# Optimization experiments

Hardware: AMD Instinct MI355X
Metric: run time of the kernel (lower is better)

The kernel has to match this reference:

```python
import jax, jax.numpy as jnp
import numpy as np


def setup_inputs() -> dict:
    key = jax.random.key(0)
    ks = jax.random.split(key, 16)
    B, T, A, R, M, D = 128, 1024, 512, 1024, 256, 256  # batch, max_time, annot, rnn, memory, attn dims
    F, K = 32, 31  # location filters, kernel size
    s = jnp.float32(0.02)
    return dict(
        memory=jax.random.normal(ks[0], (B, M), jnp.float32),
        context=jax.random.normal(ks[1], (B, A), jnp.float32),
        rnn_state=jax.random.normal(ks[2], (B, R), jnp.float32),
        annots=jax.random.normal(ks[3], (B, T, A), jnp.float32),
        atten=jax.random.uniform(ks[4], (B, 2, T), jnp.float32),
        mask=jax.random.randint(ks[5], (B, T), 0, 2).astype(jnp.int32),
        Wi=jax.random.normal(ks[6], (3 * R, A + M), jnp.float32) * s,   # GRU input weights (r,z,n)
        Wh=jax.random.normal(ks[7], (3 * R, R), jnp.float32) * s,       # GRU hidden weights
        bi=jnp.zeros((3 * R,), jnp.float32),
        bh=jnp.zeros((3 * R,), jnp.float32),
        conv_w=jax.random.normal(ks[8], (F, 2, K), jnp.float32) * s,    # loc_conv (OIH)
        loc_w=jax.random.normal(ks[9], (D, F), jnp.float32) * s,
        loc_b=jnp.zeros((D,), jnp.float32),
        q_w=jax.random.normal(ks[10], (D, R), jnp.float32) * s,
        q_b=jnp.zeros((D,), jnp.float32),
        a_w=jax.random.normal(ks[11], (D, A), jnp.float32) * s,
        a_b=jnp.zeros((D,), jnp.float32),
        v_w=jax.random.normal(ks[12], (1, D), jnp.float32) * s,
    )


def reference(memory, context, rnn_state, annots, atten, mask,
              Wi, Wh, bi, bh, conv_w, loc_w, loc_b, q_w, q_b, a_w, a_b, v_w):
    # --- GRUCell (torch gate order: r, z, n) ---
    x = jnp.concatenate([memory, context], axis=-1)          # (B, M+A)
    gi = x @ Wi.T + bi                                        # (B, 3R)
    gh = rnn_state @ Wh.T + bh                                # (B, 3R)
    ir, iz, inn = jnp.split(gi, 3, axis=-1)
    hr, hz, hn = jnp.split(gh, 3, axis=-1)
    r = jax.nn.sigmoid(ir + hr)
    z = jax.nn.sigmoid(iz + hz)
    n = jnp.tanh(inn + r * hn)
    h = (1.0 - z) * n + z * rnn_state                         # (B, R) rnn_output

    # --- Location-sensitive attention ---
    pad = (conv_w.shape[-1] - 1) // 2
    loc = jax.lax.conv_general_dilated(atten, conv_w, (1,), [(pad, pad)],
                                       dimension_numbers=('NCH', 'OIH', 'NCH'))  # (B, F, T)
    ploc = jnp.einsum('bft,df->btd', loc, loc_w) + loc_b      # (B, T, D)
    pq = (h @ q_w.T + q_b)[:, None, :]                        # (B, 1, D)
    pa = jnp.einsum('bta,da->btd', annots, a_w) + a_b         # (B, T, D)
    align = jnp.einsum('btd,d->bt', jnp.tanh(pq + pa + ploc), v_w[0])  # (B, T)

    # masked softmax (mask==0 -> -inf)
    align = jnp.where(mask != 0, align, jnp.float32(-1e30))
    align = jax.nn.softmax(align, axis=-1)

    # context = bmm(align, annots)
    ctx = jnp.einsum('bt,bta->ba', align, annots)             # (B, A)
    return (h, ctx, align)
```

## Files before the change

kernel.cpp:

```cpp
#include <hip/hip_runtime.h>
#include <cstddef>

constexpr int B  = 128;
constexpr int T  = 1024;
constexpr int AD = 512;
constexpr int R  = 1024;
constexpr int M  = 256;
constexpr int DD = 256;
constexpr int F  = 32;
constexpr int KW = 31;
constexpr int PADW = 15;
constexpr int XDIM = M + AD;
constexpr int G3 = 3 * R;
constexpr size_t BG3 = (size_t)B * G3;

using short8 = __attribute__((ext_vector_type(8))) short;
using f32x4  = __attribute__((ext_vector_type(4))) float;

__device__ __forceinline__ float sigmoidf(float x) { return 1.f / (1.f + __expf(-x)); }

__device__ __forceinline__ unsigned short f2bf(float x) {
  unsigned int u = __float_as_uint(x);
  u += 0x7FFFu + ((u >> 16) & 1u);
  return (unsigned short)(u >> 16);
}

__device__ __forceinline__ float tanh_fast(float x) {
  float e = __expf(2.f * x);
  return 1.f - 2.f / (e + 1.f);
}

__device__ __forceinline__ void load_lds16(const void* g, void* l) {
  __builtin_amdgcn_global_load_lds(
      (const __attribute__((address_space(1))) unsigned int*)g,
      (__attribute__((address_space(3))) unsigned int*)l, 16, 0, 0);
}

__global__ __launch_bounds__(256) void prep_wsw(const float* __restrict__ aw,
                                                const float* __restrict__ lw,
                                                unsigned short* __restrict__ awsw,
                                                unsigned short* __restrict__ lwsw) {
  int idx = blockIdx.x * 256 + threadIdx.x;
  int chunk = idx >> 10;
  int rn = (idx & 1023) >> 2;
  int u = idx & 3;
  int su = u ^ ((rn >> 1) & 3);
  const float* src;
  unsigned short* dst;
  if (chunk < 16) {
    src = aw + (size_t)rn * AD + chunk * 32 + u * 8;
    dst = awsw + chunk * 8192 + rn * 32 + su * 8;
  } else {
    src = lw + (size_t)rn * F + u * 8;
    dst = lwsw + rn * 32 + su * 8;
  }
  float4 f0 = *(const float4*)src;
  float4 f1 = *(const float4*)(src + 4);
  unsigned int w0 = f2bf(f0.x) | ((unsigned)f2bf(f0.y) << 16);
  unsigned int w1 = f2bf(f0.z) | ((unsigned)f2bf(f0.w) << 16);
  unsigned int w2 = f2bf(f1.x) | ((unsigned)f2bf(f1.y) << 16);
  unsigned int w3 = f2bf(f1.z) | ((unsigned)f2bf(f1.w) << 16);
  uint4 pk = {w0, w1, w2, w3};
  *(uint4*)dst = pk;
}

__global__ __launch_bounds__(256) void build_x(const float* __restrict__ mem,
                                               const float* __restrict__ ctx,
                                               float* __restrict__ x) {
  int idx = blockIdx.x * 256 + threadIdx.x;
  int b = idx / XDIM, k = idx - b * XDIM;
  x[idx] = (k < M) ? mem[(size_t)b * M + k] : ctx[(size_t)b * AD + (k - M)];
}

__global__ __launch_bounds__(256) void loc_conv(const float* __restrict__ atten,
                                                const float* __restrict__ conv_w,
                                                unsigned short* __restrict__ locw) {
  __shared__ float s_att[2 * 94];
  __shared__ float s_cw[F * 62];
  const int tid = threadIdx.x;
  const int t0 = blockIdx.x * 64, b = blockIdx.y;
  for (int i = tid; i < 2 * 94; i += 256) {
    int c = i / 94, ii = i - c * 94;
    int gt = t0 - PADW + ii;
    s_att[i] = (gt >= 0 && gt < T) ? atten[((size_t)b * 2 + c) * T + gt] : 0.f;
  }
  for (int i = tid; i < F * 62; i += 256) s_cw[i] = conv_w[i];
  __syncthreads();
  const int f = tid & 31;
  const int tb = (tid >> 5) * 8;
  float a8[8] = {0.f, 0.f, 0.f, 0.f, 0.f, 0.f, 0.f, 0.f};
#pragma unroll
  for (int c = 0; c < 2; ++c) {
    float win[38];
#pragma unroll
    for (int i = 0; i < 38; ++i) win[i] = s_att[c * 94 + tb + i];
#pragma unroll
    for (int k = 0; k < KW; ++k) {
      float w = s_cw[f * 62 + c * 31 + k];
#pragma unroll
      for (int ti = 0; ti < 8; ++ti) a8[ti] += w * win[ti + k];
    }
  }
#pragma unroll
  for (int ti = 0; ti < 8; ++ti)
    locw[((size_t)b * T + t0 + tb + ti) * F + f] = f2bf(a8[ti]);
}

__global__ __launch_bounds__(256) void gemm_fused(const float* __restrict__ x,
                                                  const float* __restrict__ rnn,
                                                  const float* __restrict__ Wi,
                                                  const float* __restrict__ Wh,
                                                  float* __restrict__ outp) {
  __shared__ __align__(16) float sX[16 * 68];
  __shared__ __align__(16) float sW[16 * 68];
  const int which = blockIdx.z >> 1, half = blockIdx.z & 1;
  const float* __restrict__ X = which ? rnn : x;
  const float* __restrict__ W = which ? Wh : Wi;
  const int K = which ? R : XDIM;
  const int Kh = K >> 1;
  const int kbeg = half * Kh, kend = kbeg + Kh;
  float* __restrict__ C = outp + (size_t)blockIdx.z * BG3;
  const int tid = threadIdx.x;
  const int g0 = blockIdx.x * 64, b0 = blockIdx.y * 64;
  const int bg = tid & 15, gg = tid >> 4;
  const int lr = tid >> 2, c4 = (tid & 3) * 4;
  float acc[4][4] = {};
  for (int k0 = kbeg; k0 < kend; k0 += 16) {
    float4 xv = *(const float4*)&X[(size_t)(b0 + lr) * K + k0 + c4];
    float4 wv = *(const float4*)&W[(size_t)(g0 + lr) * K + k0 + c4];
    sX[(c4 + 0) * 68 + lr] = xv.x; sX[(c4 + 1) * 68 + lr] = xv.y;
    sX[(c4 + 2) * 68 + lr] = xv.z; sX[(c4 + 3) * 68 + lr] = xv.w;
    sW[(c4 + 0) * 68 + lr] = wv.x; sW[(c4 + 1) * 68 + lr] = wv.y;
    sW[(c4 + 2) * 68 + lr] = wv.z; sW[(c4 + 3) * 68 + lr] = wv.w;
    __syncthreads();
#pragma unroll
    for (int k = 0; k < 16; ++k) {
      float4 xr = *(const float4*)&sX[k * 68 + bg * 4];
      float4 wr = *(const float4*)&sW[k * 68 + gg * 4];
      float xa[4] = {xr.x, xr.y, xr.z, xr.w};
      float wa[4] = {wr.x, wr.y, wr.z, wr.w};
#pragma unroll
      for (int ib = 0; ib < 4; ++ib)
#pragma unroll
        for (int jg = 0; jg < 4; ++jg) acc[ib][jg] += xa[ib] * wa[jg];
    }
    __syncthreads();
  }
#pragma unroll
  for (int ib = 0; ib < 4; ++ib) {
    float4 o;
    o.x = acc[ib][0]; o.y = acc[ib][1]; o.z = acc[ib][2]; o.w = acc[ib][3];
    *(float4*)&C[(size_t)(b0 + bg * 4 + ib) * G3 + g0 + gg * 4] = o;
  }
}

__global__ __launch_bounds__(256) void gru_combine(const float* __restrict__ gp,
                                                   const float* __restrict__ bi,
                                                   const float* __restrict__ bh,
                                                   const float* __restrict__ hprev,
                                                   float* __restrict__ hout) {
  int idx = blockIdx.x * 256 + threadIdx.x;
  int b = idx >> 10, j = idx & (R - 1);
  const float* gi0 = gp + (size_t)b * G3;
  const float* gi1 = gi0 + BG3;
  const float* gh0 = gi0 + 2 * BG3;
  const float* gh1 = gi0 + 3 * BG3;
  float ir = gi0[j] + gi1[j] + bi[j];
  float hr = gh0[j] + gh1[j] + bh[j];
  float iz = gi0[R + j] + gi1[R + j] + bi[R + j];
  float hz = gh0[R + j] + gh1[R + j] + bh[R + j];
  float inn = gi0[2 * R + j] + gi1[2 * R + j] + bi[2 * R + j];
  float hn = gh0[2 * R + j] + gh1[2 * R + j] + bh[2 * R + j];
  float r = sigmoidf(ir + hr);
  float z = sigmoidf(iz + hz);
  float n = tanhf(inn + r * hn);
  float hp = hprev[(size_t)b * R + j];
  hout[(size_t)b * R + j] = (1.f - z) * n + z * hp;
}

__global__ __launch_bounds__(256) void pq_kernel(const float* __restrict__ h,
                                                 const float* __restrict__ q_w,
                                                 const float* __restrict__ q_b,
                                                 float* __restrict__ pq) {
  __shared__ __align__(16) float sh[R];
  int b = blockIdx.x, tid = threadIdx.x;
  ((float4*)sh)[tid] = ((const float4*)(h + (size_t)b * R))[tid];
  __syncthreads();
  const float* wr = q_w + (size_t)tid * R;
  float acc = 0.f;
#pragma unroll 4
  for (int k = 0; k < R; k += 4) {
    float4 w = *(const float4*)&wr[k];
    float4 x = *(const float4*)&sh[k];
    acc += w.x * x.x + w.y * x.y + w.z * x.z + w.w * x.w;
  }
  pq[(size_t)b * DD + tid] = acc + q_b[tid];
}

__global__ __launch_bounds__(512, 4) void attn_energy_mfma(
    const float* __restrict__ annots, const unsigned short* __restrict__ locw,
    const int* __restrict__ mask,
    const unsigned short* __restrict__ awsw, const unsigned short* __restrict__ lwsw,
    const float* __restrict__ loc_b, const float* __restrict__ a_b,
    const float* __restrict__ v_w, const float* __restrict__ pq,
    float* __restrict__ align_out) {
  __shared__ __align__(16) unsigned short s_A[2][128 * 32];
  __shared__ __align__(16) unsigned short s_B[2][256 * 32];

  const int tid = threadIdx.x;
  const int wv = tid >> 6;
  const int wr = wv >> 2;
  const int wc = wv & 3;
  const int lane = tid & 63;
  const int lm = lane & 15;
  const int lg = lane >> 4;
  const int t0 = blockIdx.x * 128;
  const int b = blockIdx.y;
  const int suf = lg ^ ((lm >> 1) & 3);
  const int ar = tid >> 2, au = tid & 3;
  const int asu = au ^ ((ar >> 1) & 3);

  {
    float4 f0, f1;
    const float* gp = annots + ((size_t)b * T + t0 + ar) * AD + au * 8;
    f0 = *(const float4*)gp;
    f1 = *(const float4*)(gp + 4);
    load_lds16(awsw + (size_t)wv * 1024 + lane * 8, &s_B[0][wv * 1024]);
    load_lds16(awsw + (size_t)wv * 1024 + 512 + lane * 8, &s_B[0][wv * 1024 + 512]);
    unsigned int w0 = f2bf(f0.x) | ((unsigned)f2bf(f0.y) << 16);
    unsigned int w1 = f2bf(f0.z) | ((unsigned)f2bf(f0.w) << 16);
    unsigned int w2 = f2bf(f1.x) | ((unsigned)f2bf(f1.y) << 16);
    unsigned int w3 = f2bf(f1.z) | ((unsigned)f2bf(f1.w) << 16);
    uint4 pk = {w0, w1, w2, w3};
    *(uint4*)&s_A[0][ar * 32 + asu * 8] = pk;
  }

  f32x4 acc[4][4];
#pragma unroll
  for (int j = 0; j < 4; ++j) {
    int d = wc * 64 + j * 16 + lm;
    float base = pq[(size_t)b * DD + d] + a_b[d] + loc_b[d];
    f32x4 bv = {base, base, base, base};
#pragma unroll
    for (int i = 0; i < 4; ++i) acc[i][j] = bv;
  }
  __syncthreads();

#pragma unroll 1
  for (int ks = 0; ks < 17; ++ks) {
    const int cur = ks & 1, nxt = cur ^ 1;
    const int kn = ks + 1;
    float4 f0, f1;
    uint4 lv;
    if (kn < 16) {
      const float* gp = annots + ((size_t)b * T + t0 + ar) * AD + kn * 32 + au * 8;
      f0 = *(const float4*)gp;
      f1 = *(const float4*)(gp + 4);
      load_lds16(awsw + (size_t)kn * 8192 + wv * 1024 + lane * 8, &s_B[nxt][wv * 1024]);
      load_lds16(awsw + (size_t)kn * 8192 + wv * 1024 + 512 + lane * 8,
                 &s_B[nxt][wv * 1024 + 512]);
    } else if (kn == 16) {
      lv = *(const uint4*)(locw + ((size_t)b * T + t0 + ar) * F + au * 8);
      load_lds16(lwsw + (size_t)wv * 1024 + lane * 8, &s_B[nxt][wv * 1024]);
      load_lds16(lwsw + (size_t)wv * 1024 + 512 + lane * 8, &s_B[nxt][wv * 1024 + 512]);
    }
    short8 afr[4], bfr[4];
#pragma unroll
    for (int i = 0; i < 4; ++i)
      afr[i] = *(const short8*)&s_A[cur][(wr * 64 + i * 16 + lm) * 32 + suf * 8];
#pragma unroll
    for (int j = 0; j < 4; ++j)
      bfr[j] = *(const short8*)&s_B[cur][(wc * 64 + j * 16 + lm) * 32 + suf * 8];
#pragma unroll
    for (int j = 0; j < 4; ++j)
#pragma unroll
      for (int i = 0; i < 4; ++i)
        acc[i][j] = __builtin_amdgcn_mfma_f32_16x16x32_bf16(afr[i], bfr[j], acc[i][j], 0, 0, 0);
    if (kn < 16) {
      unsigned int w0 = f2bf(f0.x) | ((unsigned)f2bf(f0.y) << 16);
      unsigned int w1 = f2bf(f0.z) | ((unsigned)f2bf(f0.w) << 16);
      unsigned int w2 = f2bf(f1.x) | ((unsigned)f2bf(f1.y) << 16);
      unsigned int w3 = f2bf(f1.z) | ((unsigned)f2bf(f1.w) << 16);
      uint4 pk = {w0, w1, w2, w3};
      *(uint4*)&s_A[nxt][ar * 32 + asu * 8] = pk;
    } else if (kn == 16) {
      *(uint4*)&s_A[nxt][ar * 32 + asu * 8] = lv;
    }
    __syncthreads();
  }

  float vwv[4];
#pragma unroll
  for (int j = 0; j < 4; ++j) vwv[j] = v_w[wc * 64 + j * 16 + lm];
  float* s_e = (float*)s_A;
#pragma unroll
  for (int i = 0; i < 4; ++i) {
#pragma unroll
    for (int reg = 0; reg < 4; ++reg) {
      float p = 0.f;
#pragma unroll
      for (int j = 0; j < 4; ++j) p += vwv[j] * tanh_fast(acc[i][j][reg]);
      p += __shfl_xor(p, 1);
      p += __shfl_xor(p, 2);
      p += __shfl_xor(p, 4);
      p += __shfl_xor(p, 8);
      if (lm == 0) s_e[wc * 128 + wr * 64 + i * 16 + lg * 4 + reg] = p;
    }
  }
  __syncthreads();
  if (tid < 128) {
    float e = s_e[tid] + s_e[128 + tid] + s_e[256 + tid] + s_e[384 + tid];
    e = (mask[(size_t)b * T + t0 + tid] != 0) ? e : -1e30f;
    align_out[(size_t)b * T + t0 + tid] = e;
  }
}

__global__ __launch_bounds__(256) void softmax_kernel(float* __restrict__ al) {
  __shared__ float s[256];
  int b = blockIdx.x, tid = threadIdx.x;
  float4 v = *(float4*)&al[(size_t)b * T + tid * 4];
  float m = fmaxf(fmaxf(v.x, v.y), fmaxf(v.z, v.w));
  s[tid] = m;
  __syncthreads();
  for (int off = 128; off > 0; off >>= 1) {
    if (tid < off) s[tid] = fmaxf(s[tid], s[tid + off]);
    __syncthreads();
  }
  float mx = s[0];
  __syncthreads();
  float e0 = expf(v.x - mx), e1 = expf(v.y - mx), e2 = expf(v.z - mx), e3 = expf(v.w - mx);
  s[tid] = e0 + e1 + e2 + e3;
  __syncthreads();
  for (int off = 128; off > 0; off >>= 1) {
    if (tid < off) s[tid] += s[tid + off];
    __syncthreads();
  }
  float inv = 1.f / s[0];
  float4 o = make_float4(e0 * inv, e1 * inv, e2 * inv, e3 * inv);
  *(float4*)&al[(size_t)b * T + tid * 4] = o;
}

__global__ __launch_bounds__(256) void ctx_kernel(const float* __restrict__ al,
                                                  const float* __restrict__ annots,
                                                  float* __restrict__ ctx) {
  __shared__ float s_al[128];
  int b = blockIdx.x, tid = threadIdx.x;
  int tq = blockIdx.y * 128;
  if (tid < 128) s_al[tid] = al[(size_t)b * T + tq + tid];
  __syncthreads();
  const int c4 = (tid & 127) * 4;
  const int th = tid >> 7;
  float4 acc = {0.f, 0.f, 0.f, 0.f};
  for (int t = th; t < 128; t += 2) {
    float w = s_al[t];
    float4 v = *(const float4*)&annots[((size_t)b * T + tq + t) * AD + c4];
    acc.x += w * v.x; acc.y += w * v.y; acc.z += w * v.z; acc.w += w * v.w;
  }
  atomicAdd(&ctx[(size_t)b * AD + c4 + 0], acc.x);
  atomicAdd(&ctx[(size_t)b * AD + c4 + 1], acc.y);
  atomicAdd(&ctx[(size_t)b * AD + c4 + 2], acc.z);
  atomicAdd(&ctx[(size_t)b * AD + c4 + 3], acc.w);
}

extern "C" void kernel_launch(void* const* d_in, const int* in_sizes, int n_in,
                              void* d_out, int out_size, void* d_ws, size_t ws_size,
                              hipStream_t stream) {
  const float* memory = (const float*)d_in[0];
  const float* context = (const float*)d_in[1];
  const float* rnn = (const float*)d_in[2];
  const float* annots = (const float*)d_in[3];
  const float* atten = (const float*)d_in[4];
  const int* mask = (const int*)d_in[5];
  const float* Wi = (const float*)d_in[6];
  const float* Wh = (const float*)d_in[7];
  const float* bi = (const float*)d_in[8];
  const float* bh = (const float*)d_in[9];
  const float* conv_w = (const float*)d_in[10];
  const float* loc_w = (const float*)d_in[11];
  const float* loc_b = (const float*)d_in[12];
  const float* q_w = (const float*)d_in[13];
  const float* q_b = (const float*)d_in[14];
  const float* a_w = (const float*)d_in[15];
  const float* a_b = (const float*)d_in[16];
  const float* v_w = (const float*)d_in[17];

  float* out = (float*)d_out;
  float* out_h = out;
  float* out_ctx = out + (size_t)B * R;
  float* out_al = out_ctx + (size_t)B * AD;

  float* ws = (float*)d_ws;
  float* x_ws = ws;
  float* gp_ws = x_ws + (size_t)B * XDIM;
  float* pq_ws = gp_ws + 4 * BG3;
  unsigned short* awsw = (unsigned short*)(pq_ws + (size_t)B * DD);
  unsigned short* lwsw = awsw + (size_t)16 * 8192;
  unsigned short* locws = lwsw + 8192;

  prep_wsw<<<68, 256, 0, stream>>>(a_w, loc_w, awsw, lwsw);
  build_x<<<(B * XDIM) / 256, 256, 0, stream>>>(memory, context, x_ws);
  loc_conv<<<dim3(T / 64, B), 256, 0, stream>>>(atten, conv_w, locws);
  gemm_fused<<<dim3(G3 / 64, B / 64, 4), 256, 0, stream>>>(x_ws, rnn, Wi, Wh, gp_ws);
  gru_combine<<<(B * R) / 256, 256, 0, stream>>>(gp_ws, bi, bh, rnn, out_h);
  pq_kernel<<<B, 256, 0, stream>>>(out_h, q_w, q_b, pq_ws);
  attn_energy_mfma<<<dim3(T / 128, B), 512, 0, stream>>>(annots, locws, mask,
                                                         awsw, lwsw, loc_b, a_b, v_w,
                                                         pq_ws, out_al);
  softmax_kernel<<<B, 256, 0, stream>>>(out_al);
  hipMemsetAsync(out_ctx, 0, (size_t)B * AD * sizeof(float), stream);
  ctx_kernel<<<dim3(B, 8), 256, 0, stream>>>(out_al, annots, out_ctx);
}
```

Measured before the change: 222.4 us.

## Fuse attention energy, softmax and context into one kernel reusing LDS annots

The attention kernel now keeps the whole bf16 annots tile in LDS and reuses it to compute partial context sums, so the separate context pass no longer re-reads annots from global memory. Softmax is done without max subtraction, as unnormalised exponentials plus per-tile partial sums, and a small finalize kernel normalises align and ctx. The GRU GEMM now reads memory and context directly instead of going through build_x, and uses a 4-way K split with 8 partial outputs. In exchange, the large LDS footprint limits occupancy, the B-tile loads lose double buffering and gain an extra barrier, and skipping the max shift assumes the energies stay small.

```diff
diff --git a/kernel.cpp b/kernel.cpp
--- a/kernel.cpp
+++ b/kernel.cpp
@@ -64,14 +64,6 @@
   *(uint4*)dst = pk;
 }
 
-__global__ __launch_bounds__(256) void build_x(const float* __restrict__ mem,
-                                               const float* __restrict__ ctx,
-                                               float* __restrict__ x) {
-  int idx = blockIdx.x * 256 + threadIdx.x;
-  int b = idx / XDIM, k = idx - b * XDIM;
-  x[idx] = (k < M) ? mem[(size_t)b * M + k] : ctx[(size_t)b * AD + (k - M)];
-}
-
 __global__ __launch_bounds__(256) void loc_conv(const float* __restrict__ atten,
                                                 const float* __restrict__ conv_w,
                                                 unsigned short* __restrict__ locw) {
@@ -106,37 +98,42 @@
     locw[((size_t)b * T + t0 + tb + ti) * F + f] = f2bf(a8[ti]);
 }
 
-__global__ __launch_bounds__(256) void gemm_fused(const float* __restrict__ x,
-                                                  const float* __restrict__ rnn,
-                                                  const float* __restrict__ Wi,
-                                                  const float* __restrict__ Wh,
-                                                  float* __restrict__ outp) {
+__global__ __launch_bounds__(256) void gemm_fused8(const float* __restrict__ mem,
+                                                   const float* __restrict__ ctxin,
+                                                   const float* __restrict__ rnn,
+                                                   const float* __restrict__ Wi,
+                                                   const float* __restrict__ Wh,
+                                                   float* __restrict__ outp) {
   __shared__ __align__(16) float sX[16 * 68];
   __shared__ __align__(16) float sW[16 * 68];
-  const int which = blockIdx.z >> 1, half = blockIdx.z & 1;
-  const float* __restrict__ X = which ? rnn : x;
+  const int z = blockIdx.z;
+  const int which = z >> 2, q = z & 3;
   const float* __restrict__ W = which ? Wh : Wi;
   const int K = which ? R : XDIM;
-  const int Kh = K >> 1;
-  const int kbeg = half * Kh, kend = kbeg + Kh;
-  float* __restrict__ C = outp + (size_t)blockIdx.z * BG3;
+  const int Kq = K >> 2;
+  const int kbeg = q * Kq, kend = kbeg + Kq;
+  float* __restrict__ C = outp + (size_t)z * BG3;
   const int tid = threadIdx.x;
   const int g0 = blockIdx.x * 64, b0 = blockIdx.y * 64;
   const int bg = tid & 15, gg = tid >> 4;
   const int lr = tid >> 2, c4 = (tid & 3) * 4;
   float acc[4][4] = {};
   for (int k0 = kbeg; k0 < kend; k0 += 16) {
-    float4 xv = *(const float4*)&X[(size_t)(b0 + lr) * K + k0 + c4];
-    float4 wv = *(const float4*)&W[(size_t)(g0 + lr) * K + k0 + c4];
+    const int k = k0 + c4;
+    float4 xv;
+    if (which) xv = *(const float4*)&rnn[(size_t)(b0 + lr) * R + k];
+    else if (k < M) xv = *(const float4*)&mem[(size_t)(b0 + lr) * M + k];
+    else xv = *(const float4*)&ctxin[(size_t)(b0 + lr) * AD + (k - M)];
+    float4 wv = *(const float4*)&W[(size_t)(g0 + lr) * K + k];
     sX[(c4 + 0) * 68 + lr] = xv.x; sX[(c4 + 1) * 68 + lr] = xv.y;
     sX[(c4 + 2) * 68 + lr] = xv.z; sX[(c4 + 3) * 68 + lr] = xv.w;
     sW[(c4 + 0) * 68 + lr] = wv.x; sW[(c4 + 1) * 68 + lr] = wv.y;
     sW[(c4 + 2) * 68 + lr] = wv.z; sW[(c4 + 3) * 68 + lr] = wv.w;
     __syncthreads();
 #pragma unroll
-    for (int k = 0; k < 16; ++k) {
-      float4 xr = *(const float4*)&sX[k * 68 + bg * 4];
-      float4 wr = *(const float4*)&sW[k * 68 + gg * 4];
+    for (int k2 = 0; k2 < 16; ++k2) {
+      float4 xr = *(const float4*)&sX[k2 * 68 + bg * 4];
+      float4 wr = *(const float4*)&sW[k2 * 68 + gg * 4];
       float xa[4] = {xr.x, xr.y, xr.z, xr.w};
       float wa[4] = {wr.x, wr.y, wr.z, wr.w};
 #pragma unroll
@@ -161,16 +158,18 @@
                                                    float* __restrict__ hout) {
   int idx = blockIdx.x * 256 + threadIdx.x;
   int b = idx >> 10, j = idx & (R - 1);
-  const float* gi0 = gp + (size_t)b * G3;
-  const float* gi1 = gi0 + BG3;
-  const float* gh0 = gi0 + 2 * BG3;
-  const float* gh1 = gi0 + 3 * BG3;
-  float ir = gi0[j] + gi1[j] + bi[j];
-  float hr = gh0[j] + gh1[j] + bh[j];
-  float iz = gi0[R + j] + gi1[R + j] + bi[R + j];
-  float hz = gh0[R + j] + gh1[R + j] + bh[R + j];
-  float inn = gi0[2 * R + j] + gi1[2 * R + j] + bi[2 * R + j];
-  float hn = gh0[2 * R + j] + gh1[2 * R + j] + bh[2 * R + j];
+  float ir = bi[j], iz = bi[R + j], inn = bi[2 * R + j];
+  float hr = bh[j], hz = bh[R + j], hn = bh[2 * R + j];
+#pragma unroll
+  for (int z = 0; z < 4; ++z) {
+    const float* g = gp + (size_t)z * BG3 + (size_t)b * G3;
+    ir += g[j]; iz += g[R + j]; inn += g[2 * R + j];
+  }
+#pragma unroll
+  for (int z = 4; z < 8; ++z) {
+    const float* g = gp + (size_t)z * BG3 + (size_t)b * G3;
+    hr += g[j]; hz += g[R + j]; hn += g[2 * R + j];
+  }
   float r = sigmoidf(ir + hr);
   float z = sigmoidf(iz + hz);
   float n = tanhf(inn + r * hn);
@@ -197,42 +196,40 @@
   pq[(size_t)b * DD + tid] = acc + q_b[tid];
 }
 
-__global__ __launch_bounds__(512, 4) void attn_energy_mfma(
+__global__ __launch_bounds__(512, 2) void attn_fused(
     const float* __restrict__ annots, const unsigned short* __restrict__ locw,
     const int* __restrict__ mask,
     const unsigned short* __restrict__ awsw, const unsigned short* __restrict__ lwsw,
     const float* __restrict__ loc_b, const float* __restrict__ a_b,
     const float* __restrict__ v_w, const float* __restrict__ pq,
-    float* __restrict__ align_out) {
-  __shared__ __align__(16) unsigned short s_A[2][128 * 32];
-  __shared__ __align__(16) unsigned short s_B[2][256 * 32];
+    float* __restrict__ u_out, float* __restrict__ ctx_part,
+    float* __restrict__ S_part) {
+  __shared__ __align__(16) unsigned short s_Af[16 * 4096];
+  __shared__ __align__(16) unsigned short s_Al[4096];
+  __shared__ __align__(16) unsigned short s_B[8192];
 
   const int tid = threadIdx.x;
-  const int wv = tid >> 6;
-  const int wr = wv >> 2;
-  const int wc = wv & 3;
-  const int lane = tid & 63;
-  const int lm = lane & 15;
-  const int lg = lane >> 4;
-  const int t0 = blockIdx.x * 128;
-  const int b = blockIdx.y;
-  const int suf = lg ^ ((lm >> 1) & 3);
+  const int wv = tid >> 6, lane = tid & 63;
+  const int lm = lane & 15, lg = lane >> 4;
+  const int wr = wv >> 2, wc = wv & 3;
+  const int g = blockIdx.x, b = blockIdx.y;
+  const int t0 = g * 128;
   const int ar = tid >> 2, au = tid & 3;
   const int asu = au ^ ((ar >> 1) & 3);
+  const int sufb = lg ^ ((lm >> 1) & 3);
 
   {
-    float4 f0, f1;
     const float* gp = annots + ((size_t)b * T + t0 + ar) * AD + au * 8;
-    f0 = *(const float4*)gp;
-    f1 = *(const float4*)(gp + 4);
-    load_lds16(awsw + (size_t)wv * 1024 + lane * 8, &s_B[0][wv * 1024]);
-    load_lds16(awsw + (size_t)wv * 1024 + 512 + lane * 8, &s_B[0][wv * 1024 + 512]);
+    float4 f0 = *(const float4*)gp;
+    float4 f1 = *(const float4*)(gp + 4);
+    load_lds16(awsw + wv * 1024 + lane * 8, &s_B[wv * 1024]);
+    load_lds16(awsw + wv * 1024 + 512 + lane * 8, &s_B[wv * 1024 + 512]);
     unsigned int w0 = f2bf(f0.x) | ((unsigned)f2bf(f0.y) << 16);
     unsigned int w1 = f2bf(f0.z) | ((unsigned)f2bf(f0.w) << 16);
     unsigned int w2 = f2bf(f1.x) | ((unsigned)f2bf(f1.y) << 16);
     unsigned int w3 = f2bf(f1.z) | ((unsigned)f2bf(f1.w) << 16);
     uint4 pk = {w0, w1, w2, w3};
-    *(uint4*)&s_A[0][ar * 32 + asu * 8] = pk;
+    *(uint4*)&s_Af[ar * 32 + asu * 8] = pk;
   }
 
   f32x4 acc[4][4];
@@ -248,7 +245,6 @@
 
 #pragma unroll 1
   for (int ks = 0; ks < 17; ++ks) {
-    const int cur = ks & 1, nxt = cur ^ 1;
     const int kn = ks + 1;
     float4 f0, f1;
     uint4 lv;
@@ -256,21 +252,18 @@
       const float* gp = annots + ((size_t)b * T + t0 + ar) * AD + kn * 32 + au * 8;
       f0 = *(const float4*)gp;
       f1 = *(const float4*)(gp + 4);
-      load_lds16(awsw + (size_t)kn * 8192 + wv * 1024 + lane * 8, &s_B[nxt][wv * 1024]);
-      load_lds16(awsw + (size_t)kn * 8192 + wv * 1024 + 512 + lane * 8,
-                 &s_B[nxt][wv * 1024 + 512]);
     } else if (kn == 16) {
       lv = *(const uint4*)(locw + ((size_t)b * T + t0 + ar) * F + au * 8);
-      load_lds16(lwsw + (size_t)wv * 1024 + lane * 8, &s_B[nxt][wv * 1024]);
-      load_lds16(lwsw + (size_t)wv * 1024 + 512 + lane * 8, &s_B[nxt][wv * 1024 + 512]);
-    }
+    }
+    const unsigned short* As = (ks < 16) ? (s_Af + ks * 4096) : s_Al;
+    const int sfa = (ks < 16) ? (sufb ^ (ks & 3)) : sufb;
     short8 afr[4], bfr[4];
 #pragma unroll
     for (int i = 0; i < 4; ++i)
-      afr[i] = *(const short8*)&s_A[cur][(wr * 64 + i * 16 + lm) * 32 + suf * 8];
+      afr[i] = *(const short8*)&As[(wr * 64 + i * 16 + lm) * 32 + sfa * 8];
 #pragma unroll
     for (int j = 0; j < 4; ++j)
-      bfr[j] = *(const short8*)&s_B[cur][(wc * 64 + j * 16 + lm) * 32 + suf * 8];
+      bfr[j] = *(const short8*)&s_B[(wc * 64 + j * 16 + lm) * 32 + sufb * 8];
 #pragma unroll
     for (int j = 0; j < 4; ++j)
 #pragma unroll
@@ -282,17 +275,25 @@
       unsigned int w2 = f2bf(f1.x) | ((unsigned)f2bf(f1.y) << 16);
       unsigned int w3 = f2bf(f1.z) | ((unsigned)f2bf(f1.w) << 16);
       uint4 pk = {w0, w1, w2, w3};
-      *(uint4*)&s_A[nxt][ar * 32 + asu * 8] = pk;
+      *(uint4*)&s_Af[kn * 4096 + ar * 32 + (asu ^ (kn & 3)) * 8] = pk;
     } else if (kn == 16) {
-      *(uint4*)&s_A[nxt][ar * 32 + asu * 8] = lv;
+      *(uint4*)&s_Al[ar * 32 + asu * 8] = lv;
     }
     __syncthreads();
-  }
-
+    if (kn <= 16) {
+      const unsigned short* img = (kn < 16) ? (awsw + kn * 8192) : lwsw;
+      load_lds16(img + wv * 1024 + lane * 8, &s_B[wv * 1024]);
+      load_lds16(img + wv * 1024 + 512 + lane * 8, &s_B[wv * 1024 + 512]);
+      __syncthreads();
+    }
+  }
+
+  float* s_e = (float*)s_B;
+  float* s_u = s_e + 512;
+  float* s_red = s_e + 648;
   float vwv[4];
 #pragma unroll
   for (int j = 0; j < 4; ++j) vwv[j] = v_w[wc * 64 + j * 16 + lm];
-  float* s_e = (float*)s_A;
 #pragma unroll
   for (int i = 0; i < 4; ++i) {
 #pragma unroll
@@ -310,56 +311,60 @@
   __syncthreads();
   if (tid < 128) {
     float e = s_e[tid] + s_e[128 + tid] + s_e[256 + tid] + s_e[384 + tid];
-    e = (mask[(size_t)b * T + t0 + tid] != 0) ? e : -1e30f;
-    align_out[(size_t)b * T + t0 + tid] = e;
-  }
-}
-
-__global__ __launch_bounds__(256) void softmax_kernel(float* __restrict__ al) {
-  __shared__ float s[256];
+    bool mk = mask[(size_t)b * T + t0 + tid] != 0;
+    float u = mk ? __expf(e) : 0.f;
+    u_out[(size_t)b * T + t0 + tid] = u;
+    s_u[tid] = u;
+    float p = u;
+    p += __shfl_xor(p, 1);
+    p += __shfl_xor(p, 2);
+    p += __shfl_xor(p, 4);
+    p += __shfl_xor(p, 8);
+    p += __shfl_xor(p, 16);
+    p += __shfl_xor(p, 32);
+    if (lane == 0) s_red[tid >> 6] = p;
+  }
+  __syncthreads();
+  if (tid == 0) S_part[b * 8 + g] = s_red[0] + s_red[1];
+  {
+    const int cp = tid & 255, th = tid >> 8;
+    const int a0 = cp * 2;
+    const int c = a0 >> 5, uu = (a0 & 31) >> 3, ee = a0 & 7;
+    const unsigned short* base = s_Af + c * 4096;
+    float c0 = 0.f, c1 = 0.f;
+    const int tb = th * 64;
+#pragma unroll 4
+    for (int t = tb; t < tb + 64; ++t) {
+      int su = uu ^ ((t >> 1) & 3) ^ (c & 3);
+      unsigned int v = *(const unsigned int*)&base[t * 32 + su * 8 + ee];
+      float w = s_u[t];
+      c0 += w * __uint_as_float((v & 0xFFFFu) << 16);
+      c1 += w * __uint_as_float(v & 0xFFFF0000u);
+    }
+    float* dst = ctx_part + (size_t)(g * 2 + th) * ((size_t)B * AD) + (size_t)b * AD + a0;
+    dst[0] = c0;
+    dst[1] = c1;
+  }
+}
+
+__global__ __launch_bounds__(512) void finalize(const float* __restrict__ S_part,
+                                                const float* __restrict__ ctx_part,
+                                                float* __restrict__ al,
+                                                float* __restrict__ ctxo) {
   int b = blockIdx.x, tid = threadIdx.x;
-  float4 v = *(float4*)&al[(size_t)b * T + tid * 4];
-  float m = fmaxf(fmaxf(v.x, v.y), fmaxf(v.z, v.w));
-  s[tid] = m;
-  __syncthreads();
-  for (int off = 128; off > 0; off >>= 1) {
-    if (tid < off) s[tid] = fmaxf(s[tid], s[tid + off]);
-    __syncthreads();
-  }
-  float mx = s[0];
-  __syncthreads();
-  float e0 = expf(v.x - mx), e1 = expf(v.y - mx), e2 = expf(v.z - mx), e3 = expf(v.w - mx);
-  s[tid] = e0 + e1 + e2 + e3;
-  __syncthreads();
-  for (int off = 128; off > 0; off >>= 1) {
-    if (tid < off) s[tid] += s[tid + off];
-    __syncthreads();
-  }
-  float inv = 1.f / s[0];
-  float4 o = make_float4(e0 * inv, e1 * inv, e2 * inv, e3 * inv);
-  *(float4*)&al[(size_t)b * T + tid * 4] = o;
-}
-
-__global__ __launch_bounds__(256) void ctx_kernel(const float* __restrict__ al,
-                                                  const float* __restrict__ annots,
-                                                  float* __restrict__ ctx) {
-  __shared__ float s_al[128];
-  int b = blockIdx.x, tid = threadIdx.x;
-  int tq = blockIdx.y * 128;
-  if (tid < 128) s_al[tid] = al[(size_t)b * T + tq + tid];
-  __syncthreads();
-  const int c4 = (tid & 127) * 4;
-  const int th = tid >> 7;
-  float4 acc = {0.f, 0.f, 0.f, 0.f};
-  for (int t = th; t < 128; t += 2) {
-    float w = s_al[t];
-    float4 v = *(const float4*)&annots[((size_t)b * T + tq + t) * AD + c4];
-    acc.x += w * v.x; acc.y += w * v.y; acc.z += w * v.z; acc.w += w * v.w;
-  }
-  atomicAdd(&ctx[(size_t)b * AD + c4 + 0], acc.x);
-  atomicAdd(&ctx[(size_t)b * AD + c4 + 1], acc.y);
-  atomicAdd(&ctx[(size_t)b * AD + c4 + 2], acc.z);
-  atomicAdd(&ctx[(size_t)b * AD + c4 + 3], acc.w);
+  float S = 0.f;
+#pragma unroll
+  for (int g = 0; g < 8; ++g) S += S_part[b * 8 + g];
+  float inv = 1.f / S;
+  float2* ap = (float2*)(al + (size_t)b * T);
+  float2 v = ap[tid];
+  v.x *= inv; v.y *= inv;
+  ap[tid] = v;
+  float c = 0.f;
+#pragma unroll
+  for (int p = 0; p < 16; ++p)
+    c += ctx_part[(size_t)p * ((size_t)B * AD) + (size_t)b * AD + tid];
+  ctxo[(size_t)b * AD + tid] = c * inv;
 }
 
 extern "C" void kernel_launch(void* const* d_in, const int* in_sizes, int n_in,
@@ -390,23 +395,22 @@
   float* out_al = out_ctx + (size_t)B * AD;
 
   float* ws = (float*)d_ws;
-  float* x_ws = ws;
-  float* gp_ws = x_ws + (size_t)B * XDIM;
-  float* pq_ws = gp_ws + 4 * BG3;
-  unsigned short* awsw = (unsigned short*)(pq_ws + (size_t)B * DD);
+  float* gp_ws = ws;
+  float* pq_ws = gp_ws + 8 * BG3;
+  float* S_part = pq_ws + (size_t)B * DD;
+  float* ctx_part = S_part + (size_t)B * 8;
+  unsigned short* awsw = (unsigned short*)(ctx_part + (size_t)16 * B * AD);
   unsigned short* lwsw = awsw + (size_t)16 * 8192;
   unsigned short* locws = lwsw + 8192;
 
   prep_wsw<<<68, 256, 0, stream>>>(a_w, loc_w, awsw, lwsw);
-  build_x<<<(B * XDIM) / 256, 256, 0, stream>>>(memory, context, x_ws);
   loc_conv<<<dim3(T / 64, B), 256, 0, stream>>>(atten, conv_w, locws);
-  gemm_fused<<<dim3(G3 / 64, B / 64, 4), 256, 0, stream>>>(x_ws, rnn, Wi, Wh, gp_ws);
+  gemm_fused8<<<dim3(G3 / 64, B / 64, 8), 256, 0, stream>>>(memory, context, rnn,
+                                                            Wi, Wh, gp_ws);
   gru_combine<<<(B * R) / 256, 256, 0, stream>>>(gp_ws, bi, bh, rnn, out_h);
   pq_kernel<<<B, 256, 0, stream>>>(out_h, q_w, q_b, pq_ws);
-  attn_energy_mfma<<<dim3(T / 128, B), 512, 0, stream>>>(annots, locws, mask,
-                                                         awsw, lwsw, loc_b, a_b, v_w,
-                                                         pq_ws, out_al);
-  softmax_kernel<<<B, 256, 0, stream>>>(out_al);
-  hipMemsetAsync(out_ctx, 0, (size_t)B * AD * sizeof(float), stream);
-  ctx_kernel<<<dim3(B, 8), 256, 0, stream>>>(out_al, annots, out_ctx);
-}
+  attn_fused<<<dim3(8, B), 512, 0, stream>>>(annots, locws, mask, awsw, lwsw,
+                                             loc_b, a_b, v_w, pq_ws,
+                                             out_al, ctx_part, S_part);
+  finalize<<<B, 512, 0, stream>>>(S_part, ctx_part, out_al, out_ctx);
+}
```

New measurement: 227.3 us. +2.2%, slower.
